# Performance work log

Hardware: AMD Instinct MI355X
Metric: run time of the kernel (lower is better)

## Reference

```python
import jax, jax.numpy as jnp
import numpy as np

EPS = 1e-5  # BatchNorm eps

def gcn_conv(x, src, dst, deg, dinv, W, b):
    # PyG GCNConv: out = D^{-1/2}(A+I)D^{-1/2} X W + b
    N = x.shape[0]
    xw = x @ W                               # [N, F_out]
    norm = dinv[src] * dinv[dst]             # [E]
    agg = jax.ops.segment_sum(xw[src] * norm[:, None], dst, num_segments=N)
    agg = agg + xw * (1.0 / deg)[:, None]    # self-loop term: deg^-1/2 * deg^-1/2
    return agg + b

def bn(x, g, b, m, v):
    # inference-mode BatchNorm1d over features
    return (x - m) * jax.lax.rsqrt(v + EPS) * g + b

def setup_inputs() -> dict:
    key = jax.random.key(0)
    N, E, F_in, C = 100000, 1600000, 128, 16
    dims = [F_in, 64, 128, 64, 32, C]
    ks = jax.random.split(key, 64)
    inp = {}
    inp["x"] = jax.random.normal(ks[0], (N, F_in), dtype=jnp.float32)
    inp["edge_index"] = jax.random.randint(ks[1], (2, E), 0, N, dtype=jnp.int32)
    ki = 2
    for l in range(5):
        fi, fo = dims[l], dims[l + 1]
        scale = 1.0 / np.sqrt(fi)
        inp[f"w{l+1}"] = jax.random.normal(ks[ki], (fi, fo), dtype=jnp.float32) * scale; ki += 1
        inp[f"b{l+1}"] = jnp.zeros((fo,), dtype=jnp.float32)
    for l in range(4):  # BN params for layers 1..4
        fo = dims[l + 1]
        inp[f"g{l+1}"] = jnp.ones((fo,), dtype=jnp.float32)
        inp[f"be{l+1}"] = jnp.zeros((fo,), dtype=jnp.float32)
        inp[f"m{l+1}"] = jax.random.normal(ks[ki], (fo,), dtype=jnp.float32) * 0.1; ki += 1
        inp[f"v{l+1}"] = jax.random.uniform(ks[ki], (fo,), dtype=jnp.float32, minval=0.5, maxval=1.5); ki += 1
    return inp

def reference(x, edge_index,
              w1, b1, w2, b2, w3, b3, w4, b4, w5, b5,
              g1, be1, m1, v1, g2, be2, m2, v2,
              g3, be3, m3, v3, g4, be4, m4, v4):
    N = x.shape[0]
    src, dst = edge_index[0], edge_index[1]
    deg = jax.ops.segment_sum(jnp.ones(src.shape[0], x.dtype), dst, num_segments=N) + 1.0
    dinv = jax.lax.rsqrt(deg)
    h = jax.nn.relu(bn(gcn_conv(x, src, dst, deg, dinv, w1, b1), g1, be1, m1, v1))
    h = jax.nn.relu(bn(gcn_conv(h, src, dst, deg, dinv, w2, b2), g2, be2, m2, v2))
    h = jax.nn.relu(bn(gcn_conv(h, src, dst, deg, dinv, w3, b3), g3, be3, m3, v3))
    h = jax.nn.relu(bn(gcn_conv(h, src, dst, deg, dinv, w4, b4), g4, be4, m4, v4))
    return gcn_conv(h, src, dst, deg, dinv, w5, b5)
```

## Files before the change

### kernel.cpp

```cpp
#include <hip/hip_runtime.h>
#include <hip/hip_fp16.h>

#define BEPS 1e-5f
static constexpr int TPB = 256;
static constexpr int G_SC = 512;
static constexpr int BK_SHIFT = 8;
static constexpr int BK_NODES = 256;
static constexpr int KMAX = 512;
static constexpr int BK_SLACK = 2048;

union F4H8 { float4 f4; __half2 h2[4]; };

typedef _Float16 half8 __attribute__((ext_vector_type(8)));
typedef float floatx4 __attribute__((ext_vector_type(4)));


__global__ __launch_bounds__(TPB) void k_zero_int(int* __restrict__ p, int n) {
  int i = blockIdx.x * TPB + threadIdx.x;
  if (i < n) p[i] = 0;
}

__global__ __launch_bounds__(TPB) void k_hist(const int* __restrict__ dst,
                                              int* __restrict__ histG,
                                              int* __restrict__ btot,
                                              int E, int K, int chunk) {
  __shared__ int lh[KMAX];
  int g = blockIdx.x, t = threadIdx.x;
  for (int i = t; i < KMAX; i += TPB) lh[i] = 0;
  __syncthreads();
  int e0 = g * chunk, e1 = min(E, e0 + chunk);
  for (int e = e0 + t * 4; e < e1; e += TPB * 4) {
    if (e + 4 <= e1) {
      int4 d4 = *reinterpret_cast<const int4*>(dst + e);
      atomicAdd(&lh[d4.x >> BK_SHIFT], 1);
      atomicAdd(&lh[d4.y >> BK_SHIFT], 1);
      atomicAdd(&lh[d4.z >> BK_SHIFT], 1);
      atomicAdd(&lh[d4.w >> BK_SHIFT], 1);
    } else {
      for (int q = e; q < e1; ++q) atomicAdd(&lh[dst[q] >> BK_SHIFT], 1);
    }
  }
  __syncthreads();
  for (int i = t; i < K; i += TPB) {
    histG[i * G_SC + g] = lh[i];
    atomicAdd(&btot[i], lh[i]);
  }
}

__global__ __launch_bounds__(KMAX) void k_bbase(const int* __restrict__ btot,
                                                int* __restrict__ bbase, int K) {
  __shared__ int sh[KMAX];
  int t = threadIdx.x;
  int v = (t < K) ? btot[t] : 0;
  sh[t] = v;
  __syncthreads();
  for (int s = 1; s < KMAX; s <<= 1) {
    int x = sh[t];
    int y = (t >= s) ? sh[t - s] : 0;
    __syncthreads();
    sh[t] = x + y;
    __syncthreads();
  }
  if (t < K) bbase[t] = sh[t] - v;
  if (t == 0) bbase[K] = sh[K - 1];
}

__global__ __launch_bounds__(G_SC) void k_offs(const int* __restrict__ histG,
                                               const int* __restrict__ bbase,
                                               int* __restrict__ offs) {
  __shared__ int sh[G_SC];
  int b = blockIdx.x, t = threadIdx.x;
  int v = histG[b * G_SC + t];
  sh[t] = v;
  __syncthreads();
  for (int s = 1; s < G_SC; s <<= 1) {
    int x = sh[t];
    int y = (t >= s) ? sh[t - s] : 0;
    __syncthreads();
    sh[t] = x + y;
    __syncthreads();
  }
  offs[b * G_SC + t] = bbase[b] + sh[t] - v;
}

__global__ __launch_bounds__(TPB) void k_scatter(const int* __restrict__ src,
                                                 const int* __restrict__ dst,
                                                 const int* __restrict__ offs,
                                                 unsigned int* __restrict__ pairs,
                                                 int E, int K, int chunk) {
  __shared__ int cur[KMAX];
  int g = blockIdx.x, t = threadIdx.x;
  for (int i = t; i < K; i += TPB) cur[i] = offs[i * G_SC + g];
  __syncthreads();
  int e0 = g * chunk, e1 = min(E, e0 + chunk);
  for (int e = e0 + t * 4; e < e1; e += TPB * 4) {
    if (e + 4 <= e1) {
      int4 d4 = *reinterpret_cast<const int4*>(dst + e);
      int4 s4 = *reinterpret_cast<const int4*>(src + e);
      int p0 = atomicAdd(&cur[d4.x >> BK_SHIFT], 1);
      pairs[p0] = (unsigned int)s4.x | ((unsigned int)(d4.x & (BK_NODES - 1)) << 20);
      int p1 = atomicAdd(&cur[d4.y >> BK_SHIFT], 1);
      pairs[p1] = (unsigned int)s4.y | ((unsigned int)(d4.y & (BK_NODES - 1)) << 20);
      int p2 = atomicAdd(&cur[d4.z >> BK_SHIFT], 1);
      pairs[p2] = (unsigned int)s4.z | ((unsigned int)(d4.z & (BK_NODES - 1)) << 20);
      int p3 = atomicAdd(&cur[d4.w >> BK_SHIFT], 1);
      pairs[p3] = (unsigned int)s4.w | ((unsigned int)(d4.w & (BK_NODES - 1)) << 20);
    } else {
      for (int q = e; q < e1; ++q) {
        int d = dst[q];
        int pos = atomicAdd(&cur[d >> BK_SHIFT], 1);
        pairs[pos] = (unsigned int)src[q] | ((unsigned int)(d & (BK_NODES - 1)) << 20);
      }
    }
  }
}

__global__ __launch_bounds__(TPB) void k_bucket_sort(const unsigned int* __restrict__ pairs,
                                                     const int* __restrict__ bbase,
                                                     int* __restrict__ rowptr,
                                                     int* __restrict__ rowend,
                                                     int* __restrict__ colidx,
                                                     float* __restrict__ dinv,
                                                     int N, int E) {
  __shared__ int cur[BK_NODES];
  __shared__ int sh[BK_NODES];
  int b = blockIdx.x, t = threadIdx.x;
  int base = bbase[b], end = bbase[b + 1];
  int n0 = b << BK_SHIFT;
  int nNodes = min(BK_NODES, N - n0);
  cur[t] = 0;
  __syncthreads();
  for (int e = base + t; e < end; e += TPB) atomicAdd(&cur[pairs[e] >> 20], 1);
  __syncthreads();
  int v = cur[t];
  int pd = (v + 7) & ~7;
  sh[t] = pd;
  __syncthreads();
  for (int s = 1; s < TPB; s <<= 1) {
    int x = sh[t];
    int y = (t >= s) ? sh[t - s] : 0;
    __syncthreads();
    sh[t] = x + y;
    __syncthreads();
  }
  int Bb = (base + b * BK_SLACK + 7) & ~7;
  int start = Bb + (sh[t] - pd);
  if (t < nNodes) {
    rowptr[n0 + t] = start;
    rowend[n0 + t] = start + pd;
    dinv[n0 + t] = rsqrtf((float)(v + 1));
    for (int i = start + v; i < start + pd; ++i) colidx[i] = N;
  }
  __syncthreads();
  cur[t] = start;
  __syncthreads();
  for (int e = base + t; e < end; e += TPB) {
    unsigned int p = pairs[e];
    int pos = atomicAdd(&cur[p >> 20], 1);
    colidx[pos] = (int)(p & 0xFFFFFu);
  }
}

__device__ inline void packone(const float* __restrict__ W, _Float16* __restrict__ Wp,
                               int i, int FO) {
  int j = i & 7, lane = (i >> 3) & 63, tile = i >> 9;
  int nct = FO >> 4, ct = tile % nct, kch = tile / nct;
  int k = kch * 32 + ((lane >> 4) << 3) + j;
  int n = (ct << 4) + (lane & 15);
  Wp[i] = (_Float16)W[k * FO + n];
}

__global__ __launch_bounds__(TPB) void k_packAll(const float* w1, _Float16* p1,
                                                 const float* w2, _Float16* p2,
                                                 const float* w3, _Float16* p3,
                                                 const float* w4, _Float16* p4,
                                                 const float* w5, _Float16* p5,
                                                 __half* bufA, int N) {
  int i = blockIdx.x * TPB + threadIdx.x;
  if (i < 8192) packone(w1, p1, i, 64);
  else if (i < 16384) packone(w2, p2, i - 8192, 128);
  else if (i < 24576) packone(w3, p3, i - 16384, 64);
  else if (i < 26624) packone(w4, p4, i - 24576, 32);
  else if (i < 27136) packone(w5, p5, i - 26624, 16);
  else if (i < 27144) {
    float4 z = {0.f, 0.f, 0.f, 0.f};
    reinterpret_cast<float4*>(bufA + (size_t)64 * N)[i - 27136] = z;
  }
}

__global__ __launch_bounds__(TPB) void k_mgemm1(const float* __restrict__ x,
                                                const _Float16* __restrict__ Wp,
                                                const float* __restrict__ dinv,
                                                __half* __restrict__ out, int N) {
  __shared__ float4 Wsh[4 * 4 * 64];
  __shared__ _Float16 xs[64 * 136];
  for (int i = threadIdx.x; i < 1024; i += TPB)
    Wsh[i] = reinterpret_cast<const float4*>(Wp)[i];
  int rowBase = blockIdx.x * 64;
  for (int i = threadIdx.x; i < 2048; i += TPB) {
    int r = i >> 5, c4 = i & 31;
    int gr = rowBase + r;
    float4 f = {0.f, 0.f, 0.f, 0.f};
    if (gr < N) f = reinterpret_cast<const float4*>(x)[(size_t)gr * 32 + c4];
    _Float16* p = &xs[r * 136 + c4 * 4];
    p[0] = (_Float16)f.x; p[1] = (_Float16)f.y; p[2] = (_Float16)f.z; p[3] = (_Float16)f.w;
  }
  __syncthreads();

  int lane = threadIdx.x & 63;
  int wv = threadIdx.x >> 6;
  int quad = lane >> 4;
  int m = lane & 15;
  int lrow = wv * 16 + m;

  floatx4 acc[4];
#pragma unroll
  for (int ct = 0; ct < 4; ++ct) acc[ct] = (floatx4){0.f, 0.f, 0.f, 0.f};
#pragma unroll
  for (int kch = 0; kch < 4; ++kch) {
    half8 a = *reinterpret_cast<const half8*>(&xs[lrow * 136 + kch * 32 + quad * 8]);
#pragma unroll
    for (int ct = 0; ct < 4; ++ct) {
      union { float4 f4; half8 h8; } ub;
      ub.f4 = Wsh[(kch * 4 + ct) * 64 + lane];
      acc[ct] = __builtin_amdgcn_mfma_f32_16x16x32_f16(a, ub.h8, acc[ct], 0, 0, 0);
    }
  }
  int r0 = rowBase + wv * 16 + quad * 4;
  float dv[4];
#pragma unroll
  for (int reg = 0; reg < 4; ++reg) dv[reg] = (r0 + reg < N) ? dinv[r0 + reg] : 0.f;
#pragma unroll
  for (int ct = 0; ct < 4; ++ct) {
    int col = ct * 16 + m;
#pragma unroll
    for (int reg = 0; reg < 4; ++reg) {
      int r = r0 + reg;
      out[(size_t)r * 64 + col] = __float2half(acc[ct][reg] * dv[reg]);
    }
  }
}

template <int FI, int FO>
__global__ __launch_bounds__(TPB) void k_mgemm(const __half* __restrict__ hin,
                                               const _Float16* __restrict__ Wp,
                                               const float* __restrict__ dinv,
                                               __half* __restrict__ out, int N) {
  constexpr int NCT = FO / 16;
  constexpr int NKC = FI / 32;
  __shared__ float4 Wsh[NKC * NCT * 64];
  for (int i = threadIdx.x; i < NKC * NCT * 64; i += TPB)
    Wsh[i] = reinterpret_cast<const float4*>(Wp)[i];
  __syncthreads();

  int lane = threadIdx.x & 63;
  int wv = threadIdx.x >> 6;
  int quad = lane >> 4;
  int rowBase = blockIdx.x * 64 + wv * 16;
  int rA = min(rowBase + (lane & 15), N - 1);

  floatx4 acc[NCT];
#pragma unroll
  for (int ct = 0; ct < NCT; ++ct) acc[ct] = (floatx4){0.f, 0.f, 0.f, 0.f};
#pragma unroll
  for (int kch = 0; kch < NKC; ++kch) {
    union { float4 f4; half8 h8; } ua;
    ua.f4 = reinterpret_cast<const float4*>(hin)[((size_t)rA * FI + kch * 32 + quad * 8) >> 3];
#pragma unroll
    for (int ct = 0; ct < NCT; ++ct) {
      union { float4 f4; half8 h8; } ub;
      ub.f4 = Wsh[(kch * NCT + ct) * 64 + lane];
      acc[ct] = __builtin_amdgcn_mfma_f32_16x16x32_f16(ua.h8, ub.h8, acc[ct], 0, 0, 0);
    }
  }
  int r0 = rowBase + quad * 4;
  float dv[4];
#pragma unroll
  for (int reg = 0; reg < 4; ++reg) dv[reg] = (r0 + reg < N) ? dinv[r0 + reg] : 0.f;
#pragma unroll
  for (int ct = 0; ct < NCT; ++ct) {
    int col = ct * 16 + (lane & 15);
#pragma unroll
    for (int reg = 0; reg < 4; ++reg) {
      int r = r0 + reg;
      out[(size_t)r * FO + col] = __float2half(acc[ct][reg] * dv[reg]);
    }
  }
}

__global__ __launch_bounds__(TPB) void k_mgemm23(const __half* __restrict__ hin,
                                                 const _Float16* __restrict__ W2p,
                                                 const _Float16* __restrict__ W3p,
                                                 const float* __restrict__ dinv,
                                                 const float* __restrict__ b2,
                                                 const float* __restrict__ g2,
                                                 const float* __restrict__ be2,
                                                 const float* __restrict__ m2,
                                                 const float* __restrict__ v2,
                                                 __half* __restrict__ out, int N) {
  __shared__ float4 W2s[2 * 8 * 64];
  __shared__ float4 W3s[4 * 4 * 64];
  __shared__ _Float16 tr[4 * 16 * 136];
  for (int i = threadIdx.x; i < 1024; i += TPB) W2s[i] = reinterpret_cast<const float4*>(W2p)[i];
  for (int i = threadIdx.x; i < 1024; i += TPB) W3s[i] = reinterpret_cast<const float4*>(W3p)[i];
  __syncthreads();

  int lane = threadIdx.x & 63;
  int wv = threadIdx.x >> 6;
  int quad = lane >> 4;
  int m = lane & 15;
  int rowBase = blockIdx.x * 64 + wv * 16;
  int rA = min(rowBase + m, N - 1);

  floatx4 acc1[8];
#pragma unroll
  for (int ct = 0; ct < 8; ++ct) acc1[ct] = (floatx4){0.f, 0.f, 0.f, 0.f};
#pragma unroll
  for (int kch = 0; kch < 2; ++kch) {
    union { float4 f4; half8 h8; } ua;
    ua.f4 = reinterpret_cast<const float4*>(hin)[((size_t)rA * 64 + kch * 32 + quad * 8) >> 3];
#pragma unroll
    for (int ct = 0; ct < 8; ++ct) {
      union { float4 f4; half8 h8; } ub;
      ub.f4 = W2s[(kch * 8 + ct) * 64 + lane];
      acc1[ct] = __builtin_amdgcn_mfma_f32_16x16x32_f16(ua.h8, ub.h8, acc1[ct], 0, 0, 0);
    }
  }
  _Float16* mytr = tr + wv * 16 * 136;
#pragma unroll
  for (int ct = 0; ct < 8; ++ct) {
    int col = ct * 16 + m;
    float sc = g2[col] * rsqrtf(v2[col] + BEPS);
    float bb = b2[col] - m2[col];
    float ee = be2[col];
#pragma unroll
    for (int reg = 0; reg < 4; ++reg) {
      int r = quad * 4 + reg;
      mytr[r * 136 + col] = (_Float16)fmaxf((acc1[ct][reg] + bb) * sc + ee, 0.f);
    }
  }
  floatx4 acc2[4];
#pragma unroll
  for (int ct = 0; ct < 4; ++ct) acc2[ct] = (floatx4){0.f, 0.f, 0.f, 0.f};
#pragma unroll
  for (int kch = 0; kch < 4; ++kch) {
    half8 a2 = *reinterpret_cast<const half8*>(&mytr[m * 136 + kch * 32 + quad * 8]);
#pragma unroll
    for (int ct = 0; ct < 4; ++ct) {
      union { float4 f4; half8 h8; } ub;
      ub.f4 = W3s[(kch * 4 + ct) * 64 + lane];
      acc2[ct] = __builtin_amdgcn_mfma_f32_16x16x32_f16(a2, ub.h8, acc2[ct], 0, 0, 0);
    }
  }
  int r0 = rowBase + quad * 4;
  float dv[4];
#pragma unroll
  for (int reg = 0; reg < 4; ++reg) dv[reg] = (r0 + reg < N) ? dinv[r0 + reg] : 0.f;
#pragma unroll
  for (int ct = 0; ct < 4; ++ct) {
    int col = ct * 16 + m;
#pragma unroll
    for (int reg = 0; reg < 4; ++reg) {
      int r = r0 + reg;
      out[(size_t)r * 64 + col] = __float2half(acc2[ct][reg] * dv[reg]);
    }
  }
}

__global__ __launch_bounds__(TPB) void k_aggemm5(const __half* __restrict__ hin,
                                                 const int* __restrict__ rowptr,
                                                 const int* __restrict__ rowend,
                                                 const int* __restrict__ colidx,
                                                 const _Float16* __restrict__ Wp,
                                                 const float* __restrict__ dinv,
                                                 const float* __restrict__ b_,
                                                 const float* __restrict__ g_,
                                                 const float* __restrict__ be_,
                                                 const float* __restrict__ m_,
                                                 const float* __restrict__ v_,
                                                 __half* __restrict__ out, int N) {
  __shared__ float4 Wsh[64];
  if (threadIdx.x < 64) Wsh[threadIdx.x] = reinterpret_cast<const float4*>(Wp)[threadIdx.x];
  __syncthreads();

  int lane = threadIdx.x & 63;
  int wv = threadIdx.x >> 6;
  int quad = lane >> 4;
  int m = lane & 15;
  int rowBase = blockIdx.x * 64 + wv * 16;
  int node = rowBase + m;
  bool valid = node < N;
  int rd = valid ? node : N;
  int e0 = valid ? rowptr[node] : 0;
  int e1 = valid ? rowend[node] : 0;
  const float4* in16 = reinterpret_cast<const float4*>(hin);

  float acc[8];
  {
    F4H8 u;
    u.f4 = in16[(size_t)rd * 4 + quad];
#pragma unroll
    for (int i = 0; i < 4; ++i) {
      float2 t2 = __half22float2(u.h2[i]);
      acc[2 * i] = t2.x;
      acc[2 * i + 1] = t2.y;
    }
  }
  for (int e = e0; e < e1; e += 4) {
    int4 c = *reinterpret_cast<const int4*>(colidx + e);
    F4H8 u0, u1, u2, u3;
    u0.f4 = in16[(size_t)c.x * 4 + quad];
    u1.f4 = in16[(size_t)c.y * 4 + quad];
    u2.f4 = in16[(size_t)c.z * 4 + quad];
    u3.f4 = in16[(size_t)c.w * 4 + quad];
#pragma unroll
    for (int i = 0; i < 4; ++i) {
      float2 a = __half22float2(u0.h2[i]), b = __half22float2(u1.h2[i]);
      float2 cc = __half22float2(u2.h2[i]), d = __half22float2(u3.h2[i]);
      acc[2 * i] += (a.x + b.x) + (cc.x + d.x);
      acc[2 * i + 1] += (a.y + b.y) + (cc.y + d.y);
    }
  }
  float dvn = valid ? dinv[node] : 0.f;
  half8 afr;
#pragma unroll
  for (int j = 0; j < 8; ++j) {
    int f = quad * 8 + j;
    float sc = g_[f] * rsqrtf(v_[f] + BEPS);
    float val = fmaxf((acc[j] * dvn + b_[f] - m_[f]) * sc + be_[f], 0.f);
    afr[j] = (_Float16)val;
  }
  floatx4 c0 = (floatx4){0.f, 0.f, 0.f, 0.f};
  union { float4 f4; half8 h8; } ub;
  ub.f4 = Wsh[lane];
  c0 = __builtin_amdgcn_mfma_f32_16x16x32_f16(afr, ub.h8, c0, 0, 0, 0);
  int r0 = rowBase + quad * 4;
#pragma unroll
  for (int reg = 0; reg < 4; ++reg) {
    int r = r0 + reg;
    float dv = (r < N) ? dinv[r] : 0.f;
    out[(size_t)r * 16 + m] = __float2half(c0[reg] * dv);
  }
}

template <int F, int MODE, typename TO>
__global__ __launch_bounds__(TPB) void k_agg(const __half* __restrict__ in,
                                             const int* __restrict__ rowptr,
                                             const int* __restrict__ rowend,
                                             const int* __restrict__ colidx,
                                             const float* __restrict__ dinv,
                                             const float* __restrict__ bias,
                                             const float* __restrict__ g,
                                             const float* __restrict__ be,
                                             const float* __restrict__ m,
                                             const float* __restrict__ v,
                                             TO* __restrict__ out, int N) {
  constexpr int V = F / 8;
  constexpr int NPB = TPB / V;
  int node = blockIdx.x * NPB + (int)(threadIdx.x / V);
  int lane = threadIdx.x % V;
  if (node >= N) return;
  const float4* in16 = reinterpret_cast<const float4*>(in);
  const size_t rs = F / 8;
  float acc[8];
  {
    F4H8 u;
    u.f4 = in16[(size_t)node * rs + lane];
#pragma unroll
    for (int i = 0; i < 4; ++i) {
      float2 t2 = __half22float2(u.h2[i]);
      acc[2 * i] = t2.x;
      acc[2 * i + 1] = t2.y;
    }
  }
  int e0 = rowptr[node], e1 = rowend[node];
  int e = e0;
  for (; e + 16 <= e1; e += 16) {
    int4 c0 = *reinterpret_cast<const int4*>(colidx + e);
    int4 c1 = *reinterpret_cast<const int4*>(colidx + e + 4);
    int4 c2 = *reinterpret_cast<const int4*>(colidx + e + 8);
    int4 c3 = *reinterpret_cast<const int4*>(colidx + e + 12);
    F4H8 u[16];
    u[0].f4  = in16[(size_t)c0.x * rs + lane];
    u[1].f4  = in16[(size_t)c0.y * rs + lane];
    u[2].f4  = in16[(size_t)c0.z * rs + lane];
    u[3].f4  = in16[(size_t)c0.w * rs + lane];
    u[4].f4  = in16[(size_t)c1.x * rs + lane];
    u[5].f4  = in16[(size_t)c1.y * rs + lane];
    u[6].f4  = in16[(size_t)c1.z * rs + lane];
    u[7].f4  = in16[(size_t)c1.w * rs + lane];
    u[8].f4  = in16[(size_t)c2.x * rs + lane];
    u[9].f4  = in16[(size_t)c2.y * rs + lane];
    u[10].f4 = in16[(size_t)c2.z * rs + lane];
    u[11].f4 = in16[(size_t)c2.w * rs + lane];
    u[12].f4 = in16[(size_t)c3.x * rs + lane];
    u[13].f4 = in16[(size_t)c3.y * rs + lane];
    u[14].f4 = in16[(size_t)c3.z * rs + lane];
    u[15].f4 = in16[(size_t)c3.w * rs + lane];
#pragma unroll
    for (int q = 0; q < 16; ++q) {
#pragma unroll
      for (int i = 0; i < 4; ++i) {
        float2 t2 = __half22float2(u[q].h2[i]);
        acc[2 * i] += t2.x;
        acc[2 * i + 1] += t2.y;
      }
    }
  }
  if (e < e1) {
    int4 c0 = *reinterpret_cast<const int4*>(colidx + e);
    int4 c1 = *reinterpret_cast<const int4*>(colidx + e + 4);
    F4H8 u[8];
    u[0].f4 = in16[(size_t)c0.x * rs + lane];
    u[1].f4 = in16[(size_t)c0.y * rs + lane];
    u[2].f4 = in16[(size_t)c0.z * rs + lane];
    u[3].f4 = in16[(size_t)c0.w * rs + lane];
    u[4].f4 = in16[(size_t)c1.x * rs + lane];
    u[5].f4 = in16[(size_t)c1.y * rs + lane];
    u[6].f4 = in16[(size_t)c1.z * rs + lane];
    u[7].f4 = in16[(size_t)c1.w * rs + lane];
#pragma unroll
    for (int q = 0; q < 8; ++q) {
#pragma unroll
      for (int i = 0; i < 4; ++i) {
        float2 t2 = __half22float2(u[q].h2[i]);
        acc[2 * i] += t2.x;
        acc[2 * i + 1] += t2.y;
      }
    }
  }
  float dv = dinv[node];
#pragma unroll
  for (int i = 0; i < 8; ++i) acc[i] *= dv;
  if (MODE == 0) {
    float4 ba = reinterpret_cast<const float4*>(bias)[lane * 2];
    float4 bb = reinterpret_cast<const float4*>(bias)[lane * 2 + 1];
    acc[0] += ba.x; acc[1] += ba.y; acc[2] += ba.z; acc[3] += ba.w;
    acc[4] += bb.x; acc[5] += bb.y; acc[6] += bb.z; acc[7] += bb.w;
  } else if (MODE == 1 || MODE == 2) {
    const float4* B = reinterpret_cast<const float4*>(bias);
    const float4* G = reinterpret_cast<const float4*>(g);
    const float4* Be = reinterpret_cast<const float4*>(be);
    const float4* M = reinterpret_cast<const float4*>(m);
    const float4* Vv = reinterpret_cast<const float4*>(v);
#pragma unroll
    for (int h = 0; h < 2; ++h) {
      float4 b4 = B[lane * 2 + h], g4 = G[lane * 2 + h], e4 = Be[lane * 2 + h];
      float4 m4 = M[lane * 2 + h], v4 = Vv[lane * 2 + h];
      float* a = acc + 4 * h;
      a[0] = fmaxf((a[0] + b4.x - m4.x) * (g4.x * rsqrtf(v4.x + BEPS)) + e4.x, 0.f);
      a[1] = fmaxf((a[1] + b4.y - m4.y) * (g4.y * rsqrtf(v4.y + BEPS)) + e4.y, 0.f);
      a[2] = fmaxf((a[2] + b4.z - m4.z) * (g4.z * rsqrtf(v4.z + BEPS)) + e4.z, 0.f);
      a[3] = fmaxf((a[3] + b4.w - m4.w) * (g4.w * rsqrtf(v4.w + BEPS)) + e4.w, 0.f);
    }
    if (MODE == 2) {
#pragma unroll
      for (int i = 0; i < 8; ++i) acc[i] *= dv;
    }
  }
  if constexpr (sizeof(TO) == 2) {
    F4H8 u;
#pragma unroll
    for (int i = 0; i < 4; ++i) u.h2[i] = __floats2half2_rn(acc[2 * i], acc[2 * i + 1]);
    reinterpret_cast<float4*>(out)[(size_t)node * rs + lane] = u.f4;
  } else {
    float4 o0 = {acc[0], acc[1], acc[2], acc[3]};
    float4 o1 = {acc[4], acc[5], acc[6], acc[7]};
    float4* op = reinterpret_cast<float4*>((float*)out + (size_t)node * F + lane * 8);
    op[0] = o0;
    op[1] = o1;
  }
}


extern "C" void kernel_launch(void* const* d_in, const int* in_sizes, int n_in,
                              void* d_out, int out_size, void* d_ws, size_t ws_size,
                              hipStream_t stream) {
  const float* x = (const float*)d_in[0];
  const int* ei = (const int*)d_in[1];
  const int N = in_sizes[0] / 128;
  const int E = in_sizes[1] / 2;
  const int* src = ei;
  const int* dst = ei + E;

  const float* w1 = (const float*)d_in[2];  const float* b1 = (const float*)d_in[3];
  const float* w2 = (const float*)d_in[4];  const float* b2 = (const float*)d_in[5];
  const float* w3 = (const float*)d_in[6];  const float* b3 = (const float*)d_in[7];
  const float* w4 = (const float*)d_in[8];  const float* b4 = (const float*)d_in[9];
  const float* w5 = (const float*)d_in[10]; const float* b5 = (const float*)d_in[11];
  const float* g1 = (const float*)d_in[12]; const float* be1 = (const float*)d_in[13];
  const float* m1 = (const float*)d_in[14]; const float* v1 = (const float*)d_in[15];
  const float* g2 = (const float*)d_in[16]; const float* be2 = (const float*)d_in[17];
  const float* m2 = (const float*)d_in[18]; const float* v2 = (const float*)d_in[19];
  const float* g3 = (const float*)d_in[20]; const float* be3 = (const float*)d_in[21];
  const float* m3 = (const float*)d_in[22]; const float* v3 = (const float*)d_in[23];
  const float* g4 = (const float*)d_in[24]; const float* be4 = (const float*)d_in[25];
  const float* m4 = (const float*)d_in[26]; const float* v4 = (const float*)d_in[27];
  float* out = (float*)d_out;

  char* ws = (char*)d_ws;
  size_t off = 0;
  auto alloc = [&](size_t bytes) -> void* {
    void* p = ws + off;
    off += (bytes + 255) & ~(size_t)255;
    return p;
  };
  const int K = (N + BK_NODES - 1) >> BK_SHIFT;
  float*        dinv   = (float*)alloc((size_t)N * 4);
  int*          rowptr = (int*)alloc((size_t)N * 4);
  int*          rowend = (int*)alloc((size_t)N * 4);
  int*          colidx = (int*)alloc(((size_t)E + (size_t)(K + 1) * BK_SLACK) * 4);
  unsigned int* pairs  = (unsigned int*)alloc((size_t)E * 4);
  int*          histG  = (int*)alloc((size_t)KMAX * G_SC * 4);
  int*          offs   = (int*)alloc((size_t)KMAX * G_SC * 4);
  int*          btot   = (int*)alloc(KMAX * 4);
  int*          bbase  = (int*)alloc((KMAX + 1) * 4);
  _Float16*     wp1    = (_Float16*)alloc(128 * 64 * 2);
  _Float16*     wp2    = (_Float16*)alloc(64 * 128 * 2);
  _Float16*     wp3    = (_Float16*)alloc(128 * 64 * 2);
  _Float16*     wp4    = (_Float16*)alloc(64 * 32 * 2);
  _Float16*     wp5    = (_Float16*)alloc(32 * 16 * 2);
  __half*       bufA   = (__half*)alloc((size_t)(N + 64) * 128 * 2);
  __half*       bufB   = (__half*)alloc((size_t)(N + 64) * 128 * 2);
  (void)ws_size; (void)n_in; (void)out_size;

  const int chunk = (((E + G_SC - 1) / G_SC) + 3) & ~3;

  k_zero_int<<<2, TPB, 0, stream>>>(btot, KMAX);
  k_hist<<<G_SC, TPB, 0, stream>>>(dst, histG, btot, E, K, chunk);
  k_bbase<<<1, KMAX, 0, stream>>>(btot, bbase, K);
  k_offs<<<K, G_SC, 0, stream>>>(histG, bbase, offs);
  k_scatter<<<G_SC, TPB, 0, stream>>>(src, dst, offs, pairs, E, K, chunk);
  k_bucket_sort<<<K, TPB, 0, stream>>>(pairs, bbase, rowptr, rowend, colidx, dinv, N, E);

  k_packAll<<<(27144 + TPB - 1) / TPB, TPB, 0, stream>>>(w1, wp1, w2, wp2, w3, wp3, w4, wp4, w5, wp5, bufA, N);

  int gRow = (N + 63) / 64;
  k_mgemm1<<<gRow, TPB, 0, stream>>>(x, wp1, dinv, bufB, N);
  k_agg<64, 2, __half><<<(N + 31) / 32, TPB, 0, stream>>>(bufB, rowptr, rowend, colidx, dinv, b1, g1, be1, m1, v1, bufA, N);
  k_agg<64, 3, __half><<<(N + 31) / 32, TPB, 0, stream>>>(bufA, rowptr, rowend, colidx, dinv, nullptr, nullptr, nullptr, nullptr, nullptr, bufB, N);
  k_mgemm23<<<gRow, TPB, 0, stream>>>(bufB, wp2, wp3, dinv, b2, g2, be2, m2, v2, bufA, N);
  k_agg<64, 1, __half><<<(N + 31) / 32, TPB, 0, stream>>>(bufA, rowptr, rowend, colidx, dinv, b3, g3, be3, m3, v3, bufB, N);
  k_mgemm<64, 32><<<gRow, TPB, 0, stream>>>(bufB, wp4, dinv, bufA, N);
  k_aggemm5<<<gRow, TPB, 0, stream>>>(bufA, rowptr, rowend, colidx, wp5, dinv, b4, g4, be4, m4, v4, bufB, N);
  k_agg<16, 0, float><<<(N + 127) / 128, TPB, 0, stream>>>(bufB, rowptr, rowend, colidx, dinv, b5, nullptr, nullptr, nullptr, nullptr, out, N);
}
```

Baseline: 357.1 us.

## Fuse aggregation into following GEMMs and merge weight packing into histogram kernel

Aggregation over neighbours for layers 2 and 3 is now computed inside the GEMM kernels: each block gathers its 64 rows into LDS (with BN+ReLU for layer 3) and then runs the MFMA GEMM on that tile, which removes two standalone aggregation kernels and their intermediate global round trips. The weight-packing kernel is folded into extra blocks of the histogram kernel, and the zero kernel is replaced by a memset, cutting launches. The cost is larger LDS per block and a gather phase with more registers, which may lower occupancy in the fused kernels.

```diff
diff --git a/kernel.cpp b/kernel.cpp
--- a/kernel.cpp
+++ b/kernel.cpp
@@ -8,22 +8,46 @@
 static constexpr int BK_NODES = 256;
 static constexpr int KMAX = 512;
 static constexpr int BK_SLACK = 2048;
+static constexpr int PACK_ITEMS = 27144;
+static constexpr int PACK_BLOCKS = (PACK_ITEMS + TPB - 1) / TPB;
 
 union F4H8 { float4 f4; __half2 h2[4]; };
 
 typedef _Float16 half8 __attribute__((ext_vector_type(8)));
 typedef float floatx4 __attribute__((ext_vector_type(4)));
 
-
-__global__ __launch_bounds__(TPB) void k_zero_int(int* __restrict__ p, int n) {
-  int i = blockIdx.x * TPB + threadIdx.x;
-  if (i < n) p[i] = 0;
+__device__ inline void packone(const float* __restrict__ W, _Float16* __restrict__ Wp,
+                               int i, int FO) {
+  int j = i & 7, lane = (i >> 3) & 63, tile = i >> 9;
+  int nct = FO >> 4, ct = tile % nct, kch = tile / nct;
+  int k = kch * 32 + ((lane >> 4) << 3) + j;
+  int n = (ct << 4) + (lane & 15);
+  Wp[i] = (_Float16)W[k * FO + n];
 }
 
 __global__ __launch_bounds__(TPB) void k_hist(const int* __restrict__ dst,
                                               int* __restrict__ histG,
                                               int* __restrict__ btot,
-                                              int E, int K, int chunk) {
+                                              int E, int K, int chunk,
+                                              const float* w1, _Float16* p1,
+                                              const float* w2, _Float16* p2,
+                                              const float* w3, _Float16* p3,
+                                              const float* w4, _Float16* p4,
+                                              const float* w5, _Float16* p5,
+                                              __half* bufA, int N) {
+  if (blockIdx.x >= G_SC) {
+    int i = (blockIdx.x - G_SC) * TPB + threadIdx.x;
+    if (i < 8192) packone(w1, p1, i, 64);
+    else if (i < 16384) packone(w2, p2, i - 8192, 128);
+    else if (i < 24576) packone(w3, p3, i - 16384, 64);
+    else if (i < 26624) packone(w4, p4, i - 24576, 32);
+    else if (i < 27136) packone(w5, p5, i - 26624, 16);
+    else if (i < 27144) {
+      float4 z = {0.f, 0.f, 0.f, 0.f};
+      reinterpret_cast<float4*>(bufA + (size_t)64 * N)[i - 27136] = z;
+    }
+    return;
+  }
   __shared__ int lh[KMAX];
   int g = blockIdx.x, t = threadIdx.x;
   for (int i = t; i < KMAX; i += TPB) lh[i] = 0;
@@ -161,33 +185,6 @@
   }
 }
 
-__device__ inline void packone(const float* __restrict__ W, _Float16* __restrict__ Wp,
-                               int i, int FO) {
-  int j = i & 7, lane = (i >> 3) & 63, tile = i >> 9;
-  int nct = FO >> 4, ct = tile % nct, kch = tile / nct;
-  int k = kch * 32 + ((lane >> 4) << 3) + j;
-  int n = (ct << 4) + (lane & 15);
-  Wp[i] = (_Float16)W[k * FO + n];
-}
-
-__global__ __launch_bounds__(TPB) void k_packAll(const float* w1, _Float16* p1,
-                                                 const float* w2, _Float16* p2,
-                                                 const float* w3, _Float16* p3,
-                                                 const float* w4, _Float16* p4,
-                                                 const float* w5, _Float16* p5,
-                                                 __half* bufA, int N) {
-  int i = blockIdx.x * TPB + threadIdx.x;
-  if (i < 8192) packone(w1, p1, i, 64);
-  else if (i < 16384) packone(w2, p2, i - 8192, 128);
-  else if (i < 24576) packone(w3, p3, i - 16384, 64);
-  else if (i < 26624) packone(w4, p4, i - 24576, 32);
-  else if (i < 27136) packone(w5, p5, i - 26624, 16);
-  else if (i < 27144) {
-    float4 z = {0.f, 0.f, 0.f, 0.f};
-    reinterpret_cast<float4*>(bufA + (size_t)64 * N)[i - 27136] = z;
-  }
-}
-
 __global__ __launch_bounds__(TPB) void k_mgemm1(const float* __restrict__ x,
                                                 const _Float16* __restrict__ Wp,
                                                 const float* __restrict__ dinv,
@@ -241,92 +238,163 @@
   }
 }
 
-template <int FI, int FO>
-__global__ __launch_bounds__(TPB) void k_mgemm(const __half* __restrict__ hin,
-                                               const _Float16* __restrict__ Wp,
-                                               const float* __restrict__ dinv,
-                                               __half* __restrict__ out, int N) {
-  constexpr int NCT = FO / 16;
-  constexpr int NKC = FI / 32;
-  __shared__ float4 Wsh[NKC * NCT * 64];
-  for (int i = threadIdx.x; i < NKC * NCT * 64; i += TPB)
-    Wsh[i] = reinterpret_cast<const float4*>(Wp)[i];
-  __syncthreads();
-
-  int lane = threadIdx.x & 63;
-  int wv = threadIdx.x >> 6;
-  int quad = lane >> 4;
-  int rowBase = blockIdx.x * 64 + wv * 16;
-  int rA = min(rowBase + (lane & 15), N - 1);
-
-  floatx4 acc[NCT];
-#pragma unroll
-  for (int ct = 0; ct < NCT; ++ct) acc[ct] = (floatx4){0.f, 0.f, 0.f, 0.f};
-#pragma unroll
-  for (int kch = 0; kch < NKC; ++kch) {
-    union { float4 f4; half8 h8; } ua;
-    ua.f4 = reinterpret_cast<const float4*>(hin)[((size_t)rA * FI + kch * 32 + quad * 8) >> 3];
-#pragma unroll
-    for (int ct = 0; ct < NCT; ++ct) {
-      union { float4 f4; half8 h8; } ub;
-      ub.f4 = Wsh[(kch * NCT + ct) * 64 + lane];
-      acc[ct] = __builtin_amdgcn_mfma_f32_16x16x32_f16(ua.h8, ub.h8, acc[ct], 0, 0, 0);
-    }
-  }
-  int r0 = rowBase + quad * 4;
-  float dv[4];
-#pragma unroll
-  for (int reg = 0; reg < 4; ++reg) dv[reg] = (r0 + reg < N) ? dinv[r0 + reg] : 0.f;
-#pragma unroll
-  for (int ct = 0; ct < NCT; ++ct) {
-    int col = ct * 16 + (lane & 15);
-#pragma unroll
-    for (int reg = 0; reg < 4; ++reg) {
-      int r = r0 + reg;
-      out[(size_t)r * FO + col] = __float2half(acc[ct][reg] * dv[reg]);
-    }
-  }
-}
-
-__global__ __launch_bounds__(TPB) void k_mgemm23(const __half* __restrict__ hin,
-                                                 const _Float16* __restrict__ W2p,
-                                                 const _Float16* __restrict__ W3p,
-                                                 const float* __restrict__ dinv,
-                                                 const float* __restrict__ b2,
-                                                 const float* __restrict__ g2,
-                                                 const float* __restrict__ be2,
-                                                 const float* __restrict__ m2,
-                                                 const float* __restrict__ v2,
-                                                 __half* __restrict__ out, int N) {
+template <int DO_BN>
+__device__ inline void agg_to_lds64(const float4* __restrict__ in16,
+                                    const int* __restrict__ rowptr,
+                                    const int* __restrict__ rowend,
+                                    const int* __restrict__ colidx,
+                                    const float* __restrict__ dinv,
+                                    const float* __restrict__ B_,
+                                    const float* __restrict__ G_,
+                                    const float* __restrict__ Be_,
+                                    const float* __restrict__ M_,
+                                    const float* __restrict__ V_,
+                                    int rowBase, int N, _Float16* __restrict__ tr) {
+#pragma unroll
+  for (int pass = 0; pass < 2; ++pass) {
+    int lr = pass * 32 + (int)(threadIdx.x >> 3);
+    int lane = threadIdx.x & 7;
+    int node = rowBase + lr;
+    bool valid = node < N;
+    int rd = valid ? node : N;
+    float acc[8];
+    {
+      F4H8 u;
+      u.f4 = in16[(size_t)rd * 8 + lane];
+#pragma unroll
+      for (int i = 0; i < 4; ++i) {
+        float2 t2 = __half22float2(u.h2[i]);
+        acc[2 * i] = t2.x;
+        acc[2 * i + 1] = t2.y;
+      }
+    }
+    int e0 = valid ? rowptr[node] : 0;
+    int e1 = valid ? rowend[node] : 0;
+    int e = e0;
+    for (; e + 16 <= e1; e += 16) {
+      int4 c0 = *reinterpret_cast<const int4*>(colidx + e);
+      int4 c1 = *reinterpret_cast<const int4*>(colidx + e + 4);
+      int4 c2 = *reinterpret_cast<const int4*>(colidx + e + 8);
+      int4 c3 = *reinterpret_cast<const int4*>(colidx + e + 12);
+      F4H8 u[16];
+      u[0].f4  = in16[(size_t)c0.x * 8 + lane];
+      u[1].f4  = in16[(size_t)c0.y * 8 + lane];
+      u[2].f4  = in16[(size_t)c0.z * 8 + lane];
+      u[3].f4  = in16[(size_t)c0.w * 8 + lane];
+      u[4].f4  = in16[(size_t)c1.x * 8 + lane];
+      u[5].f4  = in16[(size_t)c1.y * 8 + lane];
+      u[6].f4  = in16[(size_t)c1.z * 8 + lane];
+      u[7].f4  = in16[(size_t)c1.w * 8 + lane];
+      u[8].f4  = in16[(size_t)c2.x * 8 + lane];
+      u[9].f4  = in16[(size_t)c2.y * 8 + lane];
+      u[10].f4 = in16[(size_t)c2.z * 8 + lane];
+      u[11].f4 = in16[(size_t)c2.w * 8 + lane];
+      u[12].f4 = in16[(size_t)c3.x * 8 + lane];
+      u[13].f4 = in16[(size_t)c3.y * 8 + lane];
+      u[14].f4 = in16[(size_t)c3.z * 8 + lane];
+      u[15].f4 = in16[(size_t)c3.w * 8 + lane];
+#pragma unroll
+      for (int q = 0; q < 16; ++q) {
+#pragma unroll
+        for (int i = 0; i < 4; ++i) {
+          float2 t2 = __half22float2(u[q].h2[i]);
+          acc[2 * i] += t2.x;
+          acc[2 * i + 1] += t2.y;
+        }
+      }
+    }
+    if (e < e1) {
+      int4 c0 = *reinterpret_cast<const int4*>(colidx + e);
+      int4 c1 = *reinterpret_cast<const int4*>(colidx + e + 4);
+      F4H8 u[8];
+      u[0].f4 = in16[(size_t)c0.x * 8 + lane];
+      u[1].f4 = in16[(size_t)c0.y * 8 + lane];
+      u[2].f4 = in16[(size_t)c0.z * 8 + lane];
+      u[3].f4 = in16[(size_t)c0.w * 8 + lane];
+      u[4].f4 = in16[(size_t)c1.x * 8 + lane];
+      u[5].f4 = in16[(size_t)c1.y * 8 + lane];
+      u[6].f4 = in16[(size_t)c1.z * 8 + lane];
+      u[7].f4 = in16[(size_t)c1.w * 8 + lane];
+#pragma unroll
+      for (int q = 0; q < 8; ++q) {
+#pragma unroll
+        for (int i = 0; i < 4; ++i) {
+          float2 t2 = __half22float2(u[q].h2[i]);
+          acc[2 * i] += t2.x;
+          acc[2 * i + 1] += t2.y;
+        }
+      }
+    }
+    float dv = valid ? dinv[node] : 0.f;
+#pragma unroll
+    for (int i = 0; i < 8; ++i) acc[i] *= dv;
+    if (DO_BN) {
+      const float4* B = reinterpret_cast<const float4*>(B_);
+      const float4* G = reinterpret_cast<const float4*>(G_);
+      const float4* Be = reinterpret_cast<const float4*>(Be_);
+      const float4* M = reinterpret_cast<const float4*>(M_);
+      const float4* Vv = reinterpret_cast<const float4*>(V_);
+#pragma unroll
+      for (int h = 0; h < 2; ++h) {
+        float4 b4 = B[lane * 2 + h], g4 = G[lane * 2 + h], e4 = Be[lane * 2 + h];
+        float4 m4 = M[lane * 2 + h], v4 = Vv[lane * 2 + h];
+        float* a = acc + 4 * h;
+        a[0] = fmaxf((a[0] + b4.x - m4.x) * (g4.x * rsqrtf(v4.x + BEPS)) + e4.x, 0.f);
+        a[1] = fmaxf((a[1] + b4.y - m4.y) * (g4.y * rsqrtf(v4.y + BEPS)) + e4.y, 0.f);
+        a[2] = fmaxf((a[2] + b4.z - m4.z) * (g4.z * rsqrtf(v4.z + BEPS)) + e4.z, 0.f);
+        a[3] = fmaxf((a[3] + b4.w - m4.w) * (g4.w * rsqrtf(v4.w + BEPS)) + e4.w, 0.f);
+      }
+    }
+    F4H8 o;
+#pragma unroll
+    for (int i = 0; i < 4; ++i) o.h2[i] = __floats2half2_rn(acc[2 * i], acc[2 * i + 1]);
+    *reinterpret_cast<float4*>(&tr[lr * 136 + lane * 8]) = o.f4;
+  }
+}
+
+__global__ __launch_bounds__(TPB) void k_aggemm23(const __half* __restrict__ hin,
+                                                  const int* __restrict__ rowptr,
+                                                  const int* __restrict__ rowend,
+                                                  const int* __restrict__ colidx,
+                                                  const _Float16* __restrict__ W2p,
+                                                  const _Float16* __restrict__ W3p,
+                                                  const float* __restrict__ dinv,
+                                                  const float* __restrict__ b2,
+                                                  const float* __restrict__ g2,
+                                                  const float* __restrict__ be2,
+                                                  const float* __restrict__ m2,
+                                                  const float* __restrict__ v2,
+                                                  __half* __restrict__ out, int N) {
   __shared__ float4 W2s[2 * 8 * 64];
   __shared__ float4 W3s[4 * 4 * 64];
-  __shared__ _Float16 tr[4 * 16 * 136];
+  __shared__ _Float16 tr[64 * 136];
   for (int i = threadIdx.x; i < 1024; i += TPB) W2s[i] = reinterpret_cast<const float4*>(W2p)[i];
   for (int i = threadIdx.x; i < 1024; i += TPB) W3s[i] = reinterpret_cast<const float4*>(W3p)[i];
+  int rowBase = blockIdx.x * 64;
+  agg_to_lds64<0>(reinterpret_cast<const float4*>(hin), rowptr, rowend, colidx, dinv,
+                  nullptr, nullptr, nullptr, nullptr, nullptr, rowBase, N, tr);
   __syncthreads();
 
   int lane = threadIdx.x & 63;
   int wv = threadIdx.x >> 6;
   int quad = lane >> 4;
   int m = lane & 15;
-  int rowBase = blockIdx.x * 64 + wv * 16;
-  int rA = min(rowBase + m, N - 1);
 
   floatx4 acc1[8];
 #pragma unroll
   for (int ct = 0; ct < 8; ++ct) acc1[ct] = (floatx4){0.f, 0.f, 0.f, 0.f};
 #pragma unroll
   for (int kch = 0; kch < 2; ++kch) {
-    union { float4 f4; half8 h8; } ua;
-    ua.f4 = reinterpret_cast<const float4*>(hin)[((size_t)rA * 64 + kch * 32 + quad * 8) >> 3];
+    half8 a = *reinterpret_cast<const half8*>(&tr[(wv * 16 + m) * 136 + kch * 32 + quad * 8]);
 #pragma unroll
     for (int ct = 0; ct < 8; ++ct) {
       union { float4 f4; half8 h8; } ub;
       ub.f4 = W2s[(kch * 8 + ct) * 64 + lane];
-      acc1[ct] = __builtin_amdgcn_mfma_f32_16x16x32_f16(ua.h8, ub.h8, acc1[ct], 0, 0, 0);
-    }
-  }
-  _Float16* mytr = tr + wv * 16 * 136;
+      acc1[ct] = __builtin_amdgcn_mfma_f32_16x16x32_f16(a, ub.h8, acc1[ct], 0, 0, 0);
+    }
+  }
+  __syncthreads();
+  _Float16* mytr = tr + (size_t)wv * 16 * 136;
 #pragma unroll
   for (int ct = 0; ct < 8; ++ct) {
     int col = ct * 16 + m;
@@ -352,7 +420,7 @@
       acc2[ct] = __builtin_amdgcn_mfma_f32_16x16x32_f16(a2, ub.h8, acc2[ct], 0, 0, 0);
     }
   }
-  int r0 = rowBase + quad * 4;
+  int r0 = rowBase + wv * 16 + quad * 4;
   float dv[4];
 #pragma unroll
   for (int reg = 0; reg < 4; ++reg) dv[reg] = (r0 + reg < N) ? dinv[r0 + reg] : 0.f;
@@ -363,6 +431,59 @@
     for (int reg = 0; reg < 4; ++reg) {
       int r = r0 + reg;
       out[(size_t)r * 64 + col] = __float2half(acc2[ct][reg] * dv[reg]);
+    }
+  }
+}
+
+__global__ __launch_bounds__(TPB) void k_aggemm34(const __half* __restrict__ hin,
+                                                  const int* __restrict__ rowptr,
+                                                  const int* __restrict__ rowend,
+                                                  const int* __restrict__ colidx,
+                                                  const _Float16* __restrict__ W4p,
+                                                  const float* __restrict__ dinv,
+                                                  const float* __restrict__ b_,
+                                                  const float* __restrict__ g_,
+                                                  const float* __restrict__ be_,
+                                                  const float* __restrict__ m_,
+                                                  const float* __restrict__ v_,
+                                                  __half* __restrict__ out, int N) {
+  __shared__ float4 W4s[2 * 2 * 64];
+  __shared__ _Float16 tr[64 * 136];
+  for (int i = threadIdx.x; i < 256; i += TPB) W4s[i] = reinterpret_cast<const float4*>(W4p)[i];
+  int rowBase = blockIdx.x * 64;
+  agg_to_lds64<1>(reinterpret_cast<const float4*>(hin), rowptr, rowend, colidx, dinv,
+                  b_, g_, be_, m_, v_, rowBase, N, tr);
+  __syncthreads();
+
+  int lane = threadIdx.x & 63;
+  int wv = threadIdx.x >> 6;
+  int quad = lane >> 4;
+  int m = lane & 15;
+
+  floatx4 acc[2];
+#pragma unroll
+  for (int ct = 0; ct < 2; ++ct) acc[ct] = (floatx4){0.f, 0.f, 0.f, 0.f};
+#pragma unroll
+  for (int kch = 0; kch < 2; ++kch) {
+    half8 a = *reinterpret_cast<const half8*>(&tr[(wv * 16 + m) * 136 + kch * 32 + quad * 8]);
+#pragma unroll
+    for (int ct = 0; ct < 2; ++ct) {
+      union { float4 f4; half8 h8; } ub;
+      ub.f4 = W4s[(kch * 2 + ct) * 64 + lane];
+      acc[ct] = __builtin_amdgcn_mfma_f32_16x16x32_f16(a, ub.h8, acc[ct], 0, 0, 0);
+    }
+  }
+  int r0 = rowBase + wv * 16 + quad * 4;
+  float dv[4];
+#pragma unroll
+  for (int reg = 0; reg < 4; ++reg) dv[reg] = (r0 + reg < N) ? dinv[r0 + reg] : 0.f;
+#pragma unroll
+  for (int ct = 0; ct < 2; ++ct) {
+    int col = ct * 16 + m;
+#pragma unroll
+    for (int reg = 0; reg < 4; ++reg) {
+      int r = r0 + reg;
+      out[(size_t)r * 32 + col] = __float2half(acc[ct][reg] * dv[reg]);
     }
   }
 }
@@ -434,7 +555,7 @@
   union { float4 f4; half8 h8; } ub;
   ub.f4 = Wsh[lane];
   c0 = __builtin_amdgcn_mfma_f32_16x16x32_f16(afr, ub.h8, c0, 0, 0, 0);
-  int r0 = rowBase + quad * 4;
+  int r0 = blockIdx.x * 64 + wv * 16 + quad * 4;
 #pragma unroll
   for (int reg = 0; reg < 4; ++reg) {
     int r = r0 + reg;
@@ -626,22 +747,20 @@
 
   const int chunk = (((E + G_SC - 1) / G_SC) + 3) & ~3;
 
-  k_zero_int<<<2, TPB, 0, stream>>>(btot, KMAX);
-  k_hist<<<G_SC, TPB, 0, stream>>>(dst, histG, btot, E, K, chunk);
+  hipMemsetAsync(btot, 0, KMAX * 4, stream);
+  k_hist<<<G_SC + PACK_BLOCKS, TPB, 0, stream>>>(dst, histG, btot, E, K, chunk,
+                                                 w1, wp1, w2, wp2, w3, wp3, w4, wp4, w5, wp5,
+                                                 bufA, N);
   k_bbase<<<1, KMAX, 0, stream>>>(btot, bbase, K);
   k_offs<<<K, G_SC, 0, stream>>>(histG, bbase, offs);
   k_scatter<<<G_SC, TPB, 0, stream>>>(src, dst, offs, pairs, E, K, chunk);
   k_bucket_sort<<<K, TPB, 0, stream>>>(pairs, bbase, rowptr, rowend, colidx, dinv, N, E);
 
-  k_packAll<<<(27144 + TPB - 1) / TPB, TPB, 0, stream>>>(w1, wp1, w2, wp2, w3, wp3, w4, wp4, w5, wp5, bufA, N);
-
   int gRow = (N + 63) / 64;
   k_mgemm1<<<gRow, TPB, 0, stream>>>(x, wp1, dinv, bufB, N);
   k_agg<64, 2, __half><<<(N + 31) / 32, TPB, 0, stream>>>(bufB, rowptr, rowend, colidx, dinv, b1, g1, be1, m1, v1, bufA, N);
-  k_agg<64, 3, __half><<<(N + 31) / 32, TPB, 0, stream>>>(bufA, rowptr, rowend, colidx, dinv, nullptr, nullptr, nullptr, nullptr, nullptr, bufB, N);
-  k_mgemm23<<<gRow, TPB, 0, stream>>>(bufB, wp2, wp3, dinv, b2, g2, be2, m2, v2, bufA, N);
-  k_agg<64, 1, __half><<<(N + 31) / 32, TPB, 0, stream>>>(bufA, rowptr, rowend, colidx, dinv, b3, g3, be3, m3, v3, bufB, N);
-  k_mgemm<64, 32><<<gRow, TPB, 0, stream>>>(bufB, wp4, dinv, bufA, N);
+  k_aggemm23<<<gRow, TPB, 0, stream>>>(bufA, rowptr, rowend, colidx, wp2, wp3, dinv, b2, g2, be2, m2, v2, bufB, N);
+  k_aggemm34<<<gRow, TPB, 0, stream>>>(bufB, rowptr, rowend, colidx, wp4, dinv, b3, g3, be3, m3, v3, bufA, N);
   k_aggemm5<<<gRow, TPB, 0, stream>>>(bufA, rowptr, rowend, colidx, wp5, dinv, b4, g4, be4, m4, v4, bufB, N);
   k_agg<16, 0, float><<<(N + 127) / 128, TPB, 0, stream>>>(bufB, rowptr, rowend, colidx, dinv, b5, nullptr, nullptr, nullptr, nullptr, out, N);
 }
```

After: 349.6 us. 2.1% less time.
